# Performance work log

Hardware: AMD Instinct MI355X
Metric: run time of the kernel (lower is better)

The kernel has to match this reference:

```python
import jax, jax.numpy as jnp
import numpy as np

H, W = 512, 512
N = H * W
NCLS = 4
D_BI, D_SP = 5, 2
THETA_ALPHA, THETA_BETA, THETA_GAMMA = 80.0, 0.0625, 3.0
BI_COMPAT, SP_COMPAT, COMPATIBILITY = 10.0, 3.0, -1.0
NUM_ITER = 10


def _build_lattice(feats):
    """Permutohedral lattice precompute (numpy, integer index construction).
    feats: [N, d]. Returns os [N,d+1] int32 (1-based), ws [N,d+1] float32,
    bn [d+1, M, 2] int32 (0 = missing neighbor), M."""
    feats = np.asarray(feats, np.float64)
    n, d = feats.shape
    inv_std = np.sqrt(2.0 / 3.0) * (d + 1)
    scale = inv_std / np.sqrt((np.arange(d) + 1.0) * (np.arange(d) + 2.0))
    cf = feats * scale
    # embedding matrix E: elevated = cf @ E.T lies on the hyperplane sum=0
    E = np.zeros((d + 1, d))
    E[0, :] = 1.0
    for j in range(1, d + 1):
        E[j, j:] = 1.0
        E[j, j - 1] = -j
    elevated = cf @ E.T  # [n, d+1]
    greedy = (np.rint(elevated / (d + 1)) * (d + 1)).astype(np.int64)
    diff = elevated - greedy
    idx = np.arange(d + 1)
    upper = idx[None, :] > idx[:, None]
    lower = idx[None, :] < idx[:, None]
    di = diff[:, :, None]
    dj = diff[:, None, :]
    rank = (((dj > di) & upper) | ((dj >= di) & lower)).sum(-1)
    rank = rank + greedy.sum(1, keepdims=True) // (d + 1)
    low = rank < 0
    rank = rank + np.where(low, d + 1, 0)
    greedy = greedy + np.where(low, d + 1, 0)
    high = rank > d
    rank = rank - np.where(high, d + 1, 0)
    greedy = greedy - np.where(high, d + 1, 0)
    # barycentric weights
    bary = np.zeros((n, d + 2))
    v = (elevated - greedy) / (d + 1)
    rows = np.repeat(np.arange(n), d + 1)
    np.add.at(bary, (rows, (d - rank).ravel()), v.ravel())
    np.add.at(bary, (rows, (d + 1 - rank).ravel()), -v.ravel())
    bary[:, 0] += 1.0 + bary[:, d + 1]
    ws = bary[:, : d + 1].astype(np.float32)
    # simplex vertex keys (first d coords; last is implied by zero-sum)
    keys = np.empty((n, d + 1, d), np.int64)
    for r in range(d + 1):
        keys[:, r, :] = (greedy + r - (d + 1) * (rank > d - r))[:, :d]
    flat = keys.reshape(-1, d)
    lo = flat.min(0) - (d + 1)
    hi = flat.max(0) + (d + 1)
    strides = np.cumprod(np.concatenate([[1], (hi - lo + 1)[:-1]]))
    coords = (flat - lo) @ strides
    uniq, first, inv = np.unique(coords, return_index=True, return_inverse=True)
    M = int(len(uniq))
    os_ = (inv.reshape(n, d + 1) + 1).astype(np.int32)
    ukeys = flat[first]
    bn = np.zeros((d + 1, M, 2), np.int32)
    for j in range(d + 1):
        n1 = ukeys - 1
        n2 = ukeys + 1
        if j < d:
            n1[:, j] = ukeys[:, j] + d
            n2[:, j] = ukeys[:, j] - d
        for t, nk in enumerate((n1, n2)):
            c = (nk - lo) @ strides
            pos = np.clip(np.searchsorted(uniq, c), 0, M - 1)
            bn[j, :, t] = np.where(uniq[pos] == c, pos + 1, 0)
    return os_, ws, bn, M


def setup_inputs() -> dict:
    key = jax.random.key(0)
    k1, k2 = jax.random.split(key)
    image = jax.random.uniform(k1, (H, W, 7), dtype=jnp.float32)
    unary = jax.random.normal(k2, (H, W, NCLS), dtype=jnp.float32)
    img = np.asarray(image)
    yy, xx = np.mgrid[0:H, 0:W].astype(np.float64)
    bifeat = np.concatenate(
        [(xx / THETA_ALPHA)[..., None], (yy / THETA_ALPHA)[..., None],
         img[..., :3] / THETA_BETA], axis=-1).reshape(N, D_BI)
    spfeat = np.stack([xx / THETA_GAMMA, yy / THETA_GAMMA], -1).reshape(N, D_SP)
    os_b, ws_b, bn_b, M_b = _build_lattice(bifeat)
    os_s, ws_s, bn_s, M_s = _build_lattice(spfeat)
    return {
        "unary": unary,
        "ws_bilateral": jnp.asarray(ws_b), "os_bilateral": jnp.asarray(os_b),
        "blur_neighbors_bilateral": jnp.asarray(bn_b), "M_bilateral": M_b,
        "ws_spatial": jnp.asarray(ws_s), "os_spatial": jnp.asarray(os_s),
        "blur_neighbors_spatial": jnp.asarray(bn_s), "M_spatial": M_s,
    }


def _perm_filter(values, os_, ws, bn, M, alpha):
    # values: [N, C]; splat -> blur -> slice
    d1 = os_.shape[1]
    C = values.shape[1]
    table = jnp.zeros((M + 1, C), values.dtype)  # row 0 = dummy (missing)
    table = table.at[os_.reshape(-1)].add(
        (values[:, None, :] * ws[:, :, None]).reshape(-1, C))
    for j in range(d1):  # [0.5, 1, 0.5] blur along each lattice axis
        table = table.at[1:].add(0.5 * (table[bn[j, :, 0]] + table[bn[j, :, 1]]))
    return alpha * jnp.einsum("nrc,nr->nc", table[os_], ws)


def _mean_field(unary, ws_b, os_b, bn_b, M_b, ws_s, os_s, bn_s, M_s):
    C = unary.shape[-1]
    u = unary.reshape(N, C)
    alpha_b = 1.0 / (1.0 + 2.0 ** (-D_BI))
    alpha_s = 1.0 / (1.0 + 2.0 ** (-D_SP))
    ones = jnp.ones((N, 1), u.dtype)
    inv_nb = 1.0 / (_perm_filter(ones, os_b, ws_b, bn_b, M_b, alpha_b) + 1e-20)
    inv_ns = 1.0 / (_perm_filter(ones, os_s, ws_s, bn_s, M_s, alpha_s) + 1e-20)
    Q = jax.nn.softmax(-u, axis=-1)
    for _ in range(NUM_ITER):
        msg = (BI_COMPAT * _perm_filter(Q, os_b, ws_b, bn_b, M_b, alpha_b) * inv_nb
               + SP_COMPAT * _perm_filter(Q, os_s, ws_s, bn_s, M_s, alpha_s) * inv_ns)
        Q = jax.nn.softmax(-u - COMPATIBILITY * msg, axis=-1)
    return Q.reshape(H, W, C)


def reference(unary, ws_bilateral, os_bilateral, blur_neighbors_bilateral, M_bilateral,
              ws_spatial, os_spatial, blur_neighbors_spatial, M_spatial):
    # Returns the refined marginals Q [H, W, NCLS]; the module's MAP output is
    # jnp.argmax(Q, -1) (kept soft here so fwd/bwd share one output).
    return _mean_field(unary, ws_bilateral, os_bilateral, blur_neighbors_bilateral,
                       M_bilateral, ws_spatial, os_spatial, blur_neighbors_spatial,
                       M_spatial)
```

## Files before the change

### kernel.cpp

```cpp
#include <hip/hip_runtime.h>

#define NPIX (512 * 512)
#define BLK 256

#define SCAN_T 256
#define SCAN_E 8
#define SCAN_CHUNK (SCAN_T * SCAN_E)

typedef _Float16 h4 __attribute__((ext_vector_type(4)));

constexpr float ALPHA_B = 32.0f / 33.0f;
constexpr float ALPHA_S = 0.8f;
constexpr float BI_COMPAT = 10.0f;
constexpr float SP_COMPAT = 3.0f;

__device__ __forceinline__ unsigned pack_ent(int n, float w) {
    float wc = fminf(fmaxf(w, 0.f), 1.f);
    unsigned iw = (unsigned)(wc * 16383.f + 0.5f);
    return (iw << 18) | (unsigned)n;
}
__device__ __forceinline__ int ent_pix(unsigned e) { return (int)(e & 0x3FFFFu); }
__device__ __forceinline__ float ent_w(unsigned e) {
    return (float)(e >> 18) * (1.0f / 16383.0f);
}

__device__ __forceinline__ float4 f4zero() { return make_float4(0.f, 0.f, 0.f, 0.f); }
__device__ __forceinline__ h4 h4zero() {
    h4 z; z.x = (_Float16)0.f; z.y = (_Float16)0.f; z.z = (_Float16)0.f; z.w = (_Float16)0.f;
    return z;
}

__global__ void k_softmax_init(const float4* __restrict__ u, float4* __restrict__ Q) {
    int n = blockIdx.x * BLK + threadIdx.x;
    if (n >= NPIX) return;
    float4 uu = u[n];
    float l0 = -uu.x, l1 = -uu.y, l2 = -uu.z, l3 = -uu.w;
    float m = fmaxf(fmaxf(l0, l1), fmaxf(l2, l3));
    float e0 = expf(l0 - m), e1 = expf(l1 - m), e2 = expf(l2 - m), e3 = expf(l3 - m);
    float inv = 1.0f / (e0 + e1 + e2 + e3);
    Q[n] = make_float4(e0 * inv, e1 * inv, e2 * inv, e3 * inv);
}

__global__ void k_count_softmax(const int* __restrict__ osb, const int* __restrict__ oss,
                                int* __restrict__ cntB, int* __restrict__ cntS,
                                const float4* __restrict__ u, float4* __restrict__ Q) {
    int n = blockIdx.x * BLK + threadIdx.x;
    if (n >= NPIX) return;
    float4 uu = u[n];
    float l0 = -uu.x, l1 = -uu.y, l2 = -uu.z, l3 = -uu.w;
    float m = fmaxf(fmaxf(l0, l1), fmaxf(l2, l3));
    float e0 = expf(l0 - m), e1 = expf(l1 - m), e2 = expf(l2 - m), e3 = expf(l3 - m);
    float inv = 1.0f / (e0 + e1 + e2 + e3);
    Q[n] = make_float4(e0 * inv, e1 * inv, e2 * inv, e3 * inv);
#pragma unroll
    for (int r = 0; r < 6; r++) atomicAdd(&cntB[osb[n * 6 + r]], 1);
#pragma unroll
    for (int r = 0; r < 3; r++) atomicAdd(&cntS[oss[n * 3 + r]], 1);
}

__global__ void k_chunk_sum(const int* __restrict__ counts, int V, int* __restrict__ csum) {
    __shared__ int lds[SCAN_T];
    int base = blockIdx.x * SCAN_CHUNK;
    int s = 0;
#pragma unroll
    for (int j = 0; j < SCAN_E; j++) {
        int idx = base + threadIdx.x * SCAN_E + j;
        if (idx < V) s += counts[idx];
    }
    lds[threadIdx.x] = s;
    __syncthreads();
    for (int off = SCAN_T / 2; off > 0; off >>= 1) {
        if ((int)threadIdx.x < off) lds[threadIdx.x] += lds[threadIdx.x + off];
        __syncthreads();
    }
    if (threadIdx.x == 0) csum[blockIdx.x] = lds[0];
}

__global__ void k_scan_csum(int* __restrict__ csum, int nchunks) {
    __shared__ int lds[SCAN_T];
    int carry = 0;
    for (int base = 0; base < nchunks; base += SCAN_T) {
        int idx = base + threadIdx.x;
        int v = (idx < nchunks) ? csum[idx] : 0;
        lds[threadIdx.x] = v;
        __syncthreads();
        for (int off = 1; off < SCAN_T; off <<= 1) {
            int t = ((int)threadIdx.x >= off) ? lds[threadIdx.x - off] : 0;
            __syncthreads();
            lds[threadIdx.x] += t;
            __syncthreads();
        }
        int incl = lds[threadIdx.x];
        int tile_total = lds[SCAN_T - 1];
        if (idx < nchunks) csum[idx] = incl - v + carry;
        carry += tile_total;
        __syncthreads();
    }
}

__global__ void k_chunk_scan(const int* __restrict__ counts, int V,
                             const int* __restrict__ csum, int* __restrict__ start,
                             int* __restrict__ cursor) {
    __shared__ int lds[SCAN_T];
    int base = blockIdx.x * SCAN_CHUNK;
    int local[SCAN_E];
    int s = 0;
#pragma unroll
    for (int j = 0; j < SCAN_E; j++) {
        int idx = base + threadIdx.x * SCAN_E + j;
        int c = (idx < V) ? counts[idx] : 0;
        local[j] = c;
        s += c;
    }
    lds[threadIdx.x] = s;
    __syncthreads();
    for (int off = 1; off < SCAN_T; off <<= 1) {
        int t = ((int)threadIdx.x >= off) ? lds[threadIdx.x - off] : 0;
        __syncthreads();
        lds[threadIdx.x] += t;
        __syncthreads();
    }
    int excl = lds[threadIdx.x] - s + csum[blockIdx.x];
#pragma unroll
    for (int j = 0; j < SCAN_E; j++) {
        int idx = base + threadIdx.x * SCAN_E + j;
        if (idx < V) { start[idx] = excl; cursor[idx] = excl; }
        excl += local[j];
    }
}

__global__ void k_fill_both(const int* __restrict__ osb, const float* __restrict__ wsb,
                            int* __restrict__ curB, unsigned* __restrict__ entB,
                            const int* __restrict__ oss, const float* __restrict__ wss,
                            int* __restrict__ curS, unsigned* __restrict__ entS) {
    int n = blockIdx.x * BLK + threadIdx.x;
    if (n >= NPIX) return;
#pragma unroll
    for (int r = 0; r < 6; r++) {
        int o = osb[n * 6 + r];
        int pos = atomicAdd(&curB[o], 1);
        entB[pos] = pack_ent(n, wsb[n * 6 + r]);
    }
#pragma unroll
    for (int r = 0; r < 3; r++) {
        int o = oss[n * 3 + r];
        int pos = atomicAdd(&curS[o], 1);
        entS[pos] = pack_ent(n, wss[n * 3 + r]);
    }
}

__global__ void k_gather1_both(const unsigned* __restrict__ entB, const int* __restrict__ startB,
                               int totB, int Vb, float* __restrict__ nB,
                               const unsigned* __restrict__ entS, const int* __restrict__ startS,
                               int totS, int Vs, float* __restrict__ nS) {
    int i = blockIdx.x * BLK + threadIdx.x;
    const unsigned* ent; const int* st; int tot, V, idx; float* out;
    if (i < Vb) { ent = entB; st = startB; tot = totB; V = Vb; out = nB; idx = i; }
    else {
        idx = i - Vb;
        if (idx >= Vs) return;
        ent = entS; st = startS; tot = totS; V = Vs; out = nS;
    }
    int s = st[idx];
    int e = (idx + 1 < V) ? st[idx + 1] : tot;
    float acc = 0.f;
    for (int k = s; k < e; k++) acc += ent_w(ent[k]);
    out[idx] = acc;
}

__global__ void k_gather4h_both(const unsigned* __restrict__ entB, const int* __restrict__ startB,
                                int totB, int Vb, h4* __restrict__ tB,
                                const unsigned* __restrict__ entS, const int* __restrict__ startS,
                                int totS, int Vs, h4* __restrict__ tS,
                                const float4* __restrict__ Q) {
    int i = blockIdx.x * BLK + threadIdx.x;
    const unsigned* ent; const int* st; int tot, V, idx; h4* out;
    if (i < Vb) { ent = entB; st = startB; tot = totB; V = Vb; out = tB; idx = i; }
    else {
        idx = i - Vb;
        if (idx >= Vs) return;
        ent = entS; st = startS; tot = totS; V = Vs; out = tS;
    }
    int s = st[idx];
    int e = (idx + 1 < V) ? st[idx + 1] : tot;
    float ax = 0.f, ay = 0.f, az = 0.f, aw = 0.f;
    for (int k = s; k < e; k++) {
        unsigned en = ent[k];
        float w = ent_w(en);
        float4 q = Q[ent_pix(en)];
        ax += w * q.x; ay += w * q.y; az += w * q.z; aw += w * q.w;
    }
    h4 h;
    h.x = (_Float16)ax; h.y = (_Float16)ay; h.z = (_Float16)az; h.w = (_Float16)aw;
    out[idx] = h;
}

__global__ void k_blur1(const float* __restrict__ in, float* __restrict__ out,
                        const int* __restrict__ bn, int M) {
    int i = blockIdx.x * BLK + threadIdx.x;
    if (i > M) return;
    if (i == 0) { out[0] = 0.f; return; }
    int n1 = bn[(size_t)(i - 1) * 2 + 0];
    int n2 = bn[(size_t)(i - 1) * 2 + 1];
    out[i] = in[i] + 0.5f * (in[n1] + in[n2]);
}

__global__ void k_blur1_both(const float* __restrict__ inB, float* __restrict__ outB,
                             const int* __restrict__ bnB, int Mb,
                             const float* __restrict__ inS, float* __restrict__ outS,
                             const int* __restrict__ bnS, int Ms) {
    int i = blockIdx.x * BLK + threadIdx.x;
    const float* in; float* out; const int* bn; int M, idx;
    if (i <= Mb) { in = inB; out = outB; bn = bnB; M = Mb; idx = i; }
    else {
        idx = i - (Mb + 1);
        if (idx > Ms) return;
        in = inS; out = outS; bn = bnS; M = Ms;
    }
    if (idx == 0) { out[0] = 0.f; return; }
    int n1 = bn[(size_t)(idx - 1) * 2 + 0];
    int n2 = bn[(size_t)(idx - 1) * 2 + 1];
    out[idx] = in[idx] + 0.5f * (in[n1] + in[n2]);
}

__global__ void k_blur4h(const h4* __restrict__ in, h4* __restrict__ out,
                         const int* __restrict__ bn, int M) {
    int i = blockIdx.x * BLK + threadIdx.x;
    if (i > M) return;
    if (i == 0) { out[0] = h4zero(); return; }
    int n1 = bn[(size_t)(i - 1) * 2 + 0];
    int n2 = bn[(size_t)(i - 1) * 2 + 1];
    h4 a = in[i], b = in[n1], c = in[n2];
    h4 o;
    o.x = (_Float16)((float)a.x + 0.5f * ((float)b.x + (float)c.x));
    o.y = (_Float16)((float)a.y + 0.5f * ((float)b.y + (float)c.y));
    o.z = (_Float16)((float)a.z + 0.5f * ((float)b.z + (float)c.z));
    o.w = (_Float16)((float)a.w + 0.5f * ((float)b.w + (float)c.w));
    out[i] = o;
}

__global__ void k_blur4h_both(const h4* __restrict__ inB, h4* __restrict__ outB,
                              const int* __restrict__ bnB, int Mb,
                              const h4* __restrict__ inS, h4* __restrict__ outS,
                              const int* __restrict__ bnS, int Ms) {
    int i = blockIdx.x * BLK + threadIdx.x;
    const h4* in; h4* out; const int* bn; int M, idx;
    if (i <= Mb) { in = inB; out = outB; bn = bnB; M = Mb; idx = i; }
    else {
        idx = i - (Mb + 1);
        if (idx > Ms) return;
        in = inS; out = outS; bn = bnS; M = Ms;
    }
    if (idx == 0) { out[0] = h4zero(); return; }
    int n1 = bn[(size_t)(idx - 1) * 2 + 0];
    int n2 = bn[(size_t)(idx - 1) * 2 + 1];
    h4 a = in[idx], b = in[n1], c = in[n2];
    h4 o;
    o.x = (_Float16)((float)a.x + 0.5f * ((float)b.x + (float)c.x));
    o.y = (_Float16)((float)a.y + 0.5f * ((float)b.y + (float)c.y));
    o.z = (_Float16)((float)a.z + 0.5f * ((float)b.z + (float)c.z));
    o.w = (_Float16)((float)a.w + 0.5f * ((float)b.w + (float)c.w));
    out[idx] = o;
}

__global__ void k_norm_prescale(const float* __restrict__ nTb, const float* __restrict__ wsb,
                                const int* __restrict__ osb,
                                const float* __restrict__ nTs, const float* __restrict__ wss,
                                const int* __restrict__ oss,
                                float* __restrict__ wsbp, float* __restrict__ wssp) {
    int n = blockIdx.x * BLK + threadIdx.x;
    if (n >= NPIX) return;
    float sb = 0.f;
#pragma unroll
    for (int r = 0; r < 6; r++) sb += wsb[n * 6 + r] * nTb[osb[n * 6 + r]];
    float cb = BI_COMPAT * ALPHA_B / (ALPHA_B * sb + 1e-20f);
#pragma unroll
    for (int r = 0; r < 6; r++) wsbp[n * 6 + r] = wsb[n * 6 + r] * cb;
    float ss = 0.f;
#pragma unroll
    for (int r = 0; r < 3; r++) ss += wss[n * 3 + r] * nTs[oss[n * 3 + r]];
    float cs = SP_COMPAT * ALPHA_S / (ALPHA_S * ss + 1e-20f);
#pragma unroll
    for (int r = 0; r < 3; r++) wssp[n * 3 + r] = wss[n * 3 + r] * cs;
}

__global__ void k_slice_combine_h(const float4* __restrict__ u,
                                  const h4* __restrict__ tb, const float* __restrict__ wsbp,
                                  const int* __restrict__ osb,
                                  const h4* __restrict__ ts, const float* __restrict__ wssp,
                                  const int* __restrict__ oss,
                                  float4* __restrict__ Qout) {
    int n = blockIdx.x * BLK + threadIdx.x;
    if (n >= NPIX) return;
    float4 uu = u[n];
    float l0 = -uu.x, l1 = -uu.y, l2 = -uu.z, l3 = -uu.w;
#pragma unroll
    for (int r = 0; r < 6; r++) {
        float w = wsbp[n * 6 + r];
        h4 t = tb[osb[n * 6 + r]];
        l0 += w * (float)t.x; l1 += w * (float)t.y; l2 += w * (float)t.z; l3 += w * (float)t.w;
    }
#pragma unroll
    for (int r = 0; r < 3; r++) {
        float w = wssp[n * 3 + r];
        h4 t = ts[oss[n * 3 + r]];
        l0 += w * (float)t.x; l1 += w * (float)t.y; l2 += w * (float)t.z; l3 += w * (float)t.w;
    }
    float m = fmaxf(fmaxf(l0, l1), fmaxf(l2, l3));
    float e0 = expf(l0 - m), e1 = expf(l1 - m), e2 = expf(l2 - m), e3 = expf(l3 - m);
    float inv = 1.0f / (e0 + e1 + e2 + e3);
    Qout[n] = make_float4(e0 * inv, e1 * inv, e2 * inv, e3 * inv);
}

template <int D1>
__global__ void k_splat1(const float* __restrict__ ws, const int* __restrict__ os,
                         float* __restrict__ table) {
    int n = blockIdx.x * BLK + threadIdx.x;
    if (n >= NPIX) return;
#pragma unroll
    for (int r = 0; r < D1; r++) atomicAdd(&table[os[n * D1 + r]], ws[n * D1 + r]);
}

template <int D1>
__global__ void k_splat4(const float4* __restrict__ Q, const float* __restrict__ ws,
                         const int* __restrict__ os, float* __restrict__ table) {
    int n = blockIdx.x * BLK + threadIdx.x;
    if (n >= NPIX) return;
    float4 q = Q[n];
#pragma unroll
    for (int r = 0; r < D1; r++) {
        float w = ws[n * D1 + r];
        int o = os[n * D1 + r];
        float* t = table + 4 * (size_t)o;
        atomicAdd(t + 0, q.x * w);
        atomicAdd(t + 1, q.y * w);
        atomicAdd(t + 2, q.z * w);
        atomicAdd(t + 3, q.w * w);
    }
}

__global__ void k_blur4(const float4* __restrict__ in, float4* __restrict__ out,
                        const int* __restrict__ bn, int M) {
    int i = blockIdx.x * BLK + threadIdx.x;
    if (i > M) return;
    if (i == 0) { out[0] = f4zero(); return; }
    int n1 = bn[(size_t)(i - 1) * 2 + 0];
    int n2 = bn[(size_t)(i - 1) * 2 + 1];
    float4 a = in[i], b = in[n1], c = in[n2];
    out[i] = make_float4(a.x + 0.5f * (b.x + c.x), a.y + 0.5f * (b.y + c.y),
                         a.z + 0.5f * (b.z + c.z), a.w + 0.5f * (b.w + c.w));
}

template <int D1>
__global__ void k_norm_slice(const float* __restrict__ table, const float* __restrict__ ws,
                             const int* __restrict__ os, float alpha,
                             float* __restrict__ inv_out) {
    int n = blockIdx.x * BLK + threadIdx.x;
    if (n >= NPIX) return;
    float s = 0.f;
#pragma unroll
    for (int r = 0; r < D1; r++) s += ws[n * D1 + r] * table[os[n * D1 + r]];
    inv_out[n] = 1.0f / (alpha * s + 1e-20f);
}

__global__ void k_slice_combine(const float4* __restrict__ u,
                                const float4* __restrict__ tb, const float* __restrict__ wsb,
                                const int* __restrict__ osb,
                                const float4* __restrict__ ts, const float* __restrict__ wss,
                                const int* __restrict__ oss,
                                const float* __restrict__ inv_nb,
                                const float* __restrict__ inv_ns,
                                float4* __restrict__ Qout) {
    int n = blockIdx.x * BLK + threadIdx.x;
    if (n >= NPIX) return;
    float4 ab = f4zero();
#pragma unroll
    for (int r = 0; r < 6; r++) {
        float w = wsb[n * 6 + r];
        float4 t = tb[osb[n * 6 + r]];
        ab.x += w * t.x; ab.y += w * t.y; ab.z += w * t.z; ab.w += w * t.w;
    }
    float4 as = f4zero();
#pragma unroll
    for (int r = 0; r < 3; r++) {
        float w = wss[n * 3 + r];
        float4 t = ts[oss[n * 3 + r]];
        as.x += w * t.x; as.y += w * t.y; as.z += w * t.z; as.w += w * t.w;
    }
    float cb = BI_COMPAT * ALPHA_B * inv_nb[n];
    float cs = SP_COMPAT * ALPHA_S * inv_ns[n];
    float4 uu = u[n];
    float l0 = -uu.x + cb * ab.x + cs * as.x;
    float l1 = -uu.y + cb * ab.y + cs * as.y;
    float l2 = -uu.z + cb * ab.z + cs * as.z;
    float l3 = -uu.w + cb * ab.w + cs * as.w;
    float m = fmaxf(fmaxf(l0, l1), fmaxf(l2, l3));
    float e0 = expf(l0 - m), e1 = expf(l1 - m), e2 = expf(l2 - m), e3 = expf(l3 - m);
    float inv = 1.0f / (e0 + e1 + e2 + e3);
    Qout[n] = make_float4(e0 * inv, e1 * inv, e2 * inv, e3 * inv);
}

extern "C" void kernel_launch(void* const* d_in, const int* in_sizes, int n_in,
                              void* d_out, int out_size, void* d_ws, size_t ws_size,
                              hipStream_t stream) {
    const float* unary = (const float*)d_in[0];
    const float* wsb   = (const float*)d_in[1];
    const int*   osb   = (const int*)d_in[2];
    const int*   bnb   = (const int*)d_in[3];
    const float* wss   = (const float*)d_in[5];
    const int*   oss   = (const int*)d_in[6];
    const int*   bns   = (const int*)d_in[7];
    const int Mb = in_sizes[3] / 12;
    const int Ms = in_sizes[7] / 6;
    const int Vb = Mb + 1, Vs = Ms + 1;
    const int totB = NPIX * 6, totS = NPIX * 3;

    float* Q = (float*)d_out;

    char* p = (char*)d_ws;
    auto alloc = [&](size_t nbytes) -> void* {
        void* r = (void*)p;
        p += (nbytes + 15) & ~(size_t)15;
        return r;
    };
    h4*   tAb  = (h4*)alloc((size_t)Vb * 8);
    h4*   tBb  = (h4*)alloc((size_t)Vb * 8);
    h4*   tAs  = (h4*)alloc((size_t)Vs * 8);
    h4*   tBs  = (h4*)alloc((size_t)Vs * 8);
    float* nAb = (float*)alloc((size_t)Vb * 4);
    float* nBb = (float*)alloc((size_t)Vb * 4);
    float* nAs = (float*)alloc((size_t)Vs * 4);
    float* nBs = (float*)alloc((size_t)Vs * 4);
    float* wsbp = (float*)alloc((size_t)NPIX * 6 * 4);
    float* wssp = (float*)alloc((size_t)NPIX * 3 * 4);
    int*  startB  = (int*)alloc((size_t)Vb * 4);
    int*  cursorB = (int*)alloc((size_t)Vb * 4);
    unsigned* entB = (unsigned*)alloc((size_t)totB * 4);
    int*  startS  = (int*)alloc((size_t)Vs * 4);
    int*  cursorS = (int*)alloc((size_t)Vs * 4);
    unsigned* entS = (unsigned*)alloc((size_t)totS * 4);
    int*  csum    = (int*)alloc(8192 * 4);
    size_t need = (size_t)(p - (char*)d_ws);
    bool use_gather = need <= ws_size;

    dim3 blk(BLK);
    dim3 gN((NPIX + BLK - 1) / BLK);
    dim3 gVb((Vb + BLK - 1) / BLK);
    dim3 gVBS((Vb + Vs + BLK - 1) / BLK);

    if (use_gather) {
        int nchB = (Vb + SCAN_CHUNK - 1) / SCAN_CHUNK;
        int nchS = (Vs + SCAN_CHUNK - 1) / SCAN_CHUNK;
        hipMemsetAsync(cursorB, 0, (size_t)Vb * 4, stream);
        hipMemsetAsync(cursorS, 0, (size_t)Vs * 4, stream);
        k_count_softmax<<<gN, blk, 0, stream>>>(osb, oss, cursorB, cursorS,
                                                (const float4*)unary, (float4*)Q);
        k_chunk_sum<<<dim3(nchB), dim3(SCAN_T), 0, stream>>>(cursorB, Vb, csum);
        k_scan_csum<<<dim3(1), dim3(SCAN_T), 0, stream>>>(csum, nchB);
        k_chunk_scan<<<dim3(nchB), dim3(SCAN_T), 0, stream>>>(cursorB, Vb, csum, startB, cursorB);
        k_chunk_sum<<<dim3(nchS), dim3(SCAN_T), 0, stream>>>(cursorS, Vs, csum);
        k_scan_csum<<<dim3(1), dim3(SCAN_T), 0, stream>>>(csum, nchS);
        k_chunk_scan<<<dim3(nchS), dim3(SCAN_T), 0, stream>>>(cursorS, Vs, csum, startS, cursorS);
        k_fill_both<<<gN, blk, 0, stream>>>(osb, wsb, cursorB, entB, oss, wss, cursorS, entS);

        k_gather1_both<<<gVBS, blk, 0, stream>>>(entB, startB, totB, Vb, nAb,
                                                 entS, startS, totS, Vs, nAs);
        {
            float* a = nAb; float* b = nBb;
            float* as_ = nAs; float* bs_ = nBs;
            for (int j = 0; j < 3; j++) {
                k_blur1_both<<<gVBS, blk, 0, stream>>>(a, b, bnb + (size_t)j * Mb * 2, Mb,
                                                       as_, bs_, bns + (size_t)j * Ms * 2, Ms);
                float* t = a; a = b; b = t;
                t = as_; as_ = bs_; bs_ = t;
            }
            for (int j = 3; j < 6; j++) {
                k_blur1<<<gVb, blk, 0, stream>>>(a, b, bnb + (size_t)j * Mb * 2, Mb);
                float* t = a; a = b; b = t;
            }
            k_norm_prescale<<<gN, blk, 0, stream>>>(a, wsb, osb, as_, wss, oss, wsbp, wssp);
        }

        for (int it = 0; it < 10; it++) {
            k_gather4h_both<<<gVBS, blk, 0, stream>>>(entB, startB, totB, Vb, tAb,
                                                      entS, startS, totS, Vs, tAs,
                                                      (const float4*)Q);
            h4* a = tAb; h4* b = tBb;
            h4* as_ = tAs; h4* bs_ = tBs;
            for (int j = 0; j < 3; j++) {
                k_blur4h_both<<<gVBS, blk, 0, stream>>>(a, b, bnb + (size_t)j * Mb * 2, Mb,
                                                        as_, bs_, bns + (size_t)j * Ms * 2, Ms);
                h4* t = a; a = b; b = t;
                t = as_; as_ = bs_; bs_ = t;
            }
            for (int j = 3; j < 6; j++) {
                k_blur4h<<<gVb, blk, 0, stream>>>(a, b, bnb + (size_t)j * Mb * 2, Mb);
                h4* t = a; a = b; b = t;
            }
            k_slice_combine_h<<<gN, blk, 0, stream>>>((const float4*)unary,
                                                      a, wsbp, osb, as_, wssp, oss,
                                                      (float4*)Q);
        }
    } else {
        char* q = (char*)d_ws;
        auto alloc2 = [&](size_t nbytes) -> void* {
            void* r = (void*)q;
            q += (nbytes + 15) & ~(size_t)15;
            return r;
        };
        float* fAb = (float*)alloc2((size_t)Vb * 4 * sizeof(float));
        float* fBb = (float*)alloc2((size_t)Vb * 4 * sizeof(float));
        float* fAs = (float*)alloc2((size_t)Vs * 4 * sizeof(float));
        float* fBs = (float*)alloc2((size_t)Vs * 4 * sizeof(float));
        float* inv_nb = (float*)alloc2(NPIX * sizeof(float));
        float* inv_ns = (float*)alloc2(NPIX * sizeof(float));
        dim3 gMb((Mb + 1 + BLK - 1) / BLK);
        dim3 gMs((Ms + 1 + BLK - 1) / BLK);

        hipMemsetAsync(fAb, 0, (size_t)Vb * sizeof(float), stream);
        k_splat1<6><<<gN, blk, 0, stream>>>(wsb, osb, fAb);
        {
            float* a = fAb; float* b = fBb;
            for (int j = 0; j < 6; j++) {
                k_blur1<<<gMb, blk, 0, stream>>>(a, b, bnb + (size_t)j * Mb * 2, Mb);
                float* t = a; a = b; b = t;
            }
            k_norm_slice<6><<<gN, blk, 0, stream>>>(a, wsb, osb, ALPHA_B, inv_nb);
        }
        hipMemsetAsync(fAs, 0, (size_t)Vs * sizeof(float), stream);
        k_splat1<3><<<gN, blk, 0, stream>>>(wss, oss, fAs);
        {
            float* a = fAs; float* b = fBs;
            for (int j = 0; j < 3; j++) {
                k_blur1<<<gMs, blk, 0, stream>>>(a, b, bns + (size_t)j * Ms * 2, Ms);
                float* t = a; a = b; b = t;
            }
            k_norm_slice<3><<<gN, blk, 0, stream>>>(a, wss, oss, ALPHA_S, inv_ns);
        }
        k_softmax_init<<<gN, blk, 0, stream>>>((const float4*)unary, (float4*)Q);
        for (int it = 0; it < 10; it++) {
            hipMemsetAsync(fAb, 0, (size_t)Vb * 4 * sizeof(float), stream);
            k_splat4<6><<<gN, blk, 0, stream>>>((const float4*)Q, wsb, osb, fAb);
            float* a = fAb; float* b = fBb;
            for (int j = 0; j < 6; j++) {
                k_blur4<<<gMb, blk, 0, stream>>>((const float4*)a, (float4*)b,
                                                 bnb + (size_t)j * Mb * 2, Mb);
                float* t = a; a = b; b = t;
            }
            float* finb = a;
            hipMemsetAsync(fAs, 0, (size_t)Vs * 4 * sizeof(float), stream);
            k_splat4<3><<<gN, blk, 0, stream>>>((const float4*)Q, wss, oss, fAs);
            float* as_ = fAs; float* bs_ = fBs;
            for (int j = 0; j < 3; j++) {
                k_blur4<<<gMs, blk, 0, stream>>>((const float4*)as_, (float4*)bs_,
                                                 bns + (size_t)j * Ms * 2, Ms);
                float* t = as_; as_ = bs_; bs_ = t;
            }
            float* fins = as_;
            k_slice_combine<<<gN, blk, 0, stream>>>((const float4*)unary,
                                                    (const float4*)finb, wsb, osb,
                                                    (const float4*)fins, wss, oss,
                                                    inv_nb, inv_ns, (float4*)Q);
        }
    }
}
```

Before: 1.010 ms.

## Fuse pairs of lattice blur passes via recomputation and switch blur buffers to fp32

Each kernel now applies two consecutive per-axis blurs by recomputing the first blur at the neighbor vertices. The spatial lattice applies all three of its axes in a single kernel. This drops the blur launch count per iteration from six to three and removes the intermediate buffer round trips, at the cost of redundant gathers: three times the reads for a two-axis fuse and nine times for the spatial three-axis fuse. Lattice buffers also move from fp16 to fp32, which doubles their memory traffic but removes the conversion and rounding.

```diff
diff --git a/kernel.cpp b/kernel.cpp
--- a/kernel.cpp
+++ b/kernel.cpp
@@ -6,8 +6,6 @@
 #define SCAN_T 256
 #define SCAN_E 8
 #define SCAN_CHUNK (SCAN_T * SCAN_E)
-
-typedef _Float16 h4 __attribute__((ext_vector_type(4)));
 
 constexpr float ALPHA_B = 32.0f / 33.0f;
 constexpr float ALPHA_S = 0.8f;
@@ -25,9 +23,45 @@
 }
 
 __device__ __forceinline__ float4 f4zero() { return make_float4(0.f, 0.f, 0.f, 0.f); }
-__device__ __forceinline__ h4 h4zero() {
-    h4 z; z.x = (_Float16)0.f; z.y = (_Float16)0.f; z.z = (_Float16)0.f; z.w = (_Float16)0.f;
-    return z;
+
+__device__ __forceinline__ float4 f4_eval1(const float4* __restrict__ t,
+                                           const int* __restrict__ bn, int x) {
+    int b1 = bn[2 * (x - 1)], b2 = bn[2 * (x - 1) + 1];
+    float4 a = t[x], u = t[b1], v = t[b2];
+    return make_float4(a.x + 0.5f * (u.x + v.x),
+                       a.y + 0.5f * (u.y + v.y),
+                       a.z + 0.5f * (u.z + v.z),
+                       a.w + 0.5f * (u.w + v.w));
+}
+__device__ __forceinline__ float4 f4_eval2(const float4* __restrict__ t,
+                                           const int* __restrict__ bnA,
+                                           const int* __restrict__ bnB, int x) {
+    int a1 = bnB[2 * (x - 1)], a2 = bnB[2 * (x - 1) + 1];
+    float4 r = f4_eval1(t, bnA, x);
+    if (a1) {
+        float4 q = f4_eval1(t, bnA, a1);
+        r.x += 0.5f * q.x; r.y += 0.5f * q.y; r.z += 0.5f * q.z; r.w += 0.5f * q.w;
+    }
+    if (a2) {
+        float4 q = f4_eval1(t, bnA, a2);
+        r.x += 0.5f * q.x; r.y += 0.5f * q.y; r.z += 0.5f * q.z; r.w += 0.5f * q.w;
+    }
+    return r;
+}
+
+__device__ __forceinline__ float f_eval1(const float* __restrict__ t,
+                                         const int* __restrict__ bn, int x) {
+    int b1 = bn[2 * (x - 1)], b2 = bn[2 * (x - 1) + 1];
+    return t[x] + 0.5f * (t[b1] + t[b2]);
+}
+__device__ __forceinline__ float f_eval2(const float* __restrict__ t,
+                                         const int* __restrict__ bnA,
+                                         const int* __restrict__ bnB, int x) {
+    int a1 = bnB[2 * (x - 1)], a2 = bnB[2 * (x - 1) + 1];
+    float r = f_eval1(t, bnA, x);
+    if (a1) r += 0.5f * f_eval1(t, bnA, a1);
+    if (a2) r += 0.5f * f_eval1(t, bnA, a2);
+    return r;
 }
 
 __global__ void k_softmax_init(const float4* __restrict__ u, float4* __restrict__ Q) {
@@ -168,13 +202,13 @@
     out[idx] = acc;
 }
 
-__global__ void k_gather4h_both(const unsigned* __restrict__ entB, const int* __restrict__ startB,
-                                int totB, int Vb, h4* __restrict__ tB,
+__global__ void k_gather4f_both(const unsigned* __restrict__ entB, const int* __restrict__ startB,
+                                int totB, int Vb, float4* __restrict__ tB,
                                 const unsigned* __restrict__ entS, const int* __restrict__ startS,
-                                int totS, int Vs, h4* __restrict__ tS,
+                                int totS, int Vs, float4* __restrict__ tS,
                                 const float4* __restrict__ Q) {
     int i = blockIdx.x * BLK + threadIdx.x;
-    const unsigned* ent; const int* st; int tot, V, idx; h4* out;
+    const unsigned* ent; const int* st; int tot, V, idx; float4* out;
     if (i < Vb) { ent = entB; st = startB; tot = totB; V = Vb; out = tB; idx = i; }
     else {
         idx = i - Vb;
@@ -183,84 +217,82 @@
     }
     int s = st[idx];
     int e = (idx + 1 < V) ? st[idx + 1] : tot;
-    float ax = 0.f, ay = 0.f, az = 0.f, aw = 0.f;
+    float4 acc = f4zero();
     for (int k = s; k < e; k++) {
         unsigned en = ent[k];
         float w = ent_w(en);
         float4 q = Q[ent_pix(en)];
-        ax += w * q.x; ay += w * q.y; az += w * q.z; aw += w * q.w;
-    }
-    h4 h;
-    h.x = (_Float16)ax; h.y = (_Float16)ay; h.z = (_Float16)az; h.w = (_Float16)aw;
-    out[idx] = h;
-}
-
-__global__ void k_blur1(const float* __restrict__ in, float* __restrict__ out,
-                        const int* __restrict__ bn, int M) {
+        acc.x += w * q.x; acc.y += w * q.y; acc.z += w * q.z; acc.w += w * q.w;
+    }
+    out[idx] = acc;
+}
+
+__global__ void k_cblur4f_both(const float4* __restrict__ inB, float4* __restrict__ outB,
+                               const int* __restrict__ bnb, int Mb,
+                               const float4* __restrict__ inS, float4* __restrict__ outS,
+                               const int* __restrict__ bns, int Ms) {
+    int i = blockIdx.x * BLK + threadIdx.x;
+    if (i <= Mb) {
+        if (i == 0) { outB[0] = f4zero(); return; }
+        outB[i] = f4_eval2(inB, bnb, bnb + (size_t)Mb * 2, i);
+        return;
+    }
+    int idx = i - (Mb + 1);
+    if (idx > Ms) return;
+    if (idx == 0) { outS[0] = f4zero(); return; }
+    const int* sn0 = bns;
+    const int* sn1 = bns + (size_t)Ms * 2;
+    const int* sn2 = bns + (size_t)Ms * 4;
+    int c1 = sn2[2 * (idx - 1)], c2 = sn2[2 * (idx - 1) + 1];
+    float4 r = f4_eval2(inS, sn0, sn1, idx);
+    if (c1) {
+        float4 q = f4_eval2(inS, sn0, sn1, c1);
+        r.x += 0.5f * q.x; r.y += 0.5f * q.y; r.z += 0.5f * q.z; r.w += 0.5f * q.w;
+    }
+    if (c2) {
+        float4 q = f4_eval2(inS, sn0, sn1, c2);
+        r.x += 0.5f * q.x; r.y += 0.5f * q.y; r.z += 0.5f * q.z; r.w += 0.5f * q.w;
+    }
+    outS[idx] = r;
+}
+
+__global__ void k_cblur4f(const float4* __restrict__ in, float4* __restrict__ out,
+                          const int* __restrict__ bnA, const int* __restrict__ bnB_, int M) {
+    int i = blockIdx.x * BLK + threadIdx.x;
+    if (i > M) return;
+    if (i == 0) { out[0] = f4zero(); return; }
+    out[i] = f4_eval2(in, bnA, bnB_, i);
+}
+
+__global__ void k_cblur1_both(const float* __restrict__ inB, float* __restrict__ outB,
+                              const int* __restrict__ bnb, int Mb,
+                              const float* __restrict__ inS, float* __restrict__ outS,
+                              const int* __restrict__ bns, int Ms) {
+    int i = blockIdx.x * BLK + threadIdx.x;
+    if (i <= Mb) {
+        if (i == 0) { outB[0] = 0.f; return; }
+        outB[i] = f_eval2(inB, bnb, bnb + (size_t)Mb * 2, i);
+        return;
+    }
+    int idx = i - (Mb + 1);
+    if (idx > Ms) return;
+    if (idx == 0) { outS[0] = 0.f; return; }
+    const int* sn0 = bns;
+    const int* sn1 = bns + (size_t)Ms * 2;
+    const int* sn2 = bns + (size_t)Ms * 4;
+    int c1 = sn2[2 * (idx - 1)], c2 = sn2[2 * (idx - 1) + 1];
+    float r = f_eval2(inS, sn0, sn1, idx);
+    if (c1) r += 0.5f * f_eval2(inS, sn0, sn1, c1);
+    if (c2) r += 0.5f * f_eval2(inS, sn0, sn1, c2);
+    outS[idx] = r;
+}
+
+__global__ void k_cblur1(const float* __restrict__ in, float* __restrict__ out,
+                         const int* __restrict__ bnA, const int* __restrict__ bnB_, int M) {
     int i = blockIdx.x * BLK + threadIdx.x;
     if (i > M) return;
     if (i == 0) { out[0] = 0.f; return; }
-    int n1 = bn[(size_t)(i - 1) * 2 + 0];
-    int n2 = bn[(size_t)(i - 1) * 2 + 1];
-    out[i] = in[i] + 0.5f * (in[n1] + in[n2]);
-}
-
-__global__ void k_blur1_both(const float* __restrict__ inB, float* __restrict__ outB,
-                             const int* __restrict__ bnB, int Mb,
-                             const float* __restrict__ inS, float* __restrict__ outS,
-                             const int* __restrict__ bnS, int Ms) {
-    int i = blockIdx.x * BLK + threadIdx.x;
-    const float* in; float* out; const int* bn; int M, idx;
-    if (i <= Mb) { in = inB; out = outB; bn = bnB; M = Mb; idx = i; }
-    else {
-        idx = i - (Mb + 1);
-        if (idx > Ms) return;
-        in = inS; out = outS; bn = bnS; M = Ms;
-    }
-    if (idx == 0) { out[0] = 0.f; return; }
-    int n1 = bn[(size_t)(idx - 1) * 2 + 0];
-    int n2 = bn[(size_t)(idx - 1) * 2 + 1];
-    out[idx] = in[idx] + 0.5f * (in[n1] + in[n2]);
-}
-
-__global__ void k_blur4h(const h4* __restrict__ in, h4* __restrict__ out,
-                         const int* __restrict__ bn, int M) {
-    int i = blockIdx.x * BLK + threadIdx.x;
-    if (i > M) return;
-    if (i == 0) { out[0] = h4zero(); return; }
-    int n1 = bn[(size_t)(i - 1) * 2 + 0];
-    int n2 = bn[(size_t)(i - 1) * 2 + 1];
-    h4 a = in[i], b = in[n1], c = in[n2];
-    h4 o;
-    o.x = (_Float16)((float)a.x + 0.5f * ((float)b.x + (float)c.x));
-    o.y = (_Float16)((float)a.y + 0.5f * ((float)b.y + (float)c.y));
-    o.z = (_Float16)((float)a.z + 0.5f * ((float)b.z + (float)c.z));
-    o.w = (_Float16)((float)a.w + 0.5f * ((float)b.w + (float)c.w));
-    out[i] = o;
-}
-
-__global__ void k_blur4h_both(const h4* __restrict__ inB, h4* __restrict__ outB,
-                              const int* __restrict__ bnB, int Mb,
-                              const h4* __restrict__ inS, h4* __restrict__ outS,
-                              const int* __restrict__ bnS, int Ms) {
-    int i = blockIdx.x * BLK + threadIdx.x;
-    const h4* in; h4* out; const int* bn; int M, idx;
-    if (i <= Mb) { in = inB; out = outB; bn = bnB; M = Mb; idx = i; }
-    else {
-        idx = i - (Mb + 1);
-        if (idx > Ms) return;
-        in = inS; out = outS; bn = bnS; M = Ms;
-    }
-    if (idx == 0) { out[0] = h4zero(); return; }
-    int n1 = bn[(size_t)(idx - 1) * 2 + 0];
-    int n2 = bn[(size_t)(idx - 1) * 2 + 1];
-    h4 a = in[idx], b = in[n1], c = in[n2];
-    h4 o;
-    o.x = (_Float16)((float)a.x + 0.5f * ((float)b.x + (float)c.x));
-    o.y = (_Float16)((float)a.y + 0.5f * ((float)b.y + (float)c.y));
-    o.z = (_Float16)((float)a.z + 0.5f * ((float)b.z + (float)c.z));
-    o.w = (_Float16)((float)a.w + 0.5f * ((float)b.w + (float)c.w));
-    out[idx] = o;
+    out[i] = f_eval2(in, bnA, bnB_, i);
 }
 
 __global__ void k_norm_prescale(const float* __restrict__ nTb, const float* __restrict__ wsb,
@@ -284,10 +316,10 @@
     for (int r = 0; r < 3; r++) wssp[n * 3 + r] = wss[n * 3 + r] * cs;
 }
 
-__global__ void k_slice_combine_h(const float4* __restrict__ u,
-                                  const h4* __restrict__ tb, const float* __restrict__ wsbp,
+__global__ void k_slice_combine_f(const float4* __restrict__ u,
+                                  const float4* __restrict__ tb, const float* __restrict__ wsbp,
                                   const int* __restrict__ osb,
-                                  const h4* __restrict__ ts, const float* __restrict__ wssp,
+                                  const float4* __restrict__ ts, const float* __restrict__ wssp,
                                   const int* __restrict__ oss,
                                   float4* __restrict__ Qout) {
     int n = blockIdx.x * BLK + threadIdx.x;
@@ -297,14 +329,14 @@
 #pragma unroll
     for (int r = 0; r < 6; r++) {
         float w = wsbp[n * 6 + r];
-        h4 t = tb[osb[n * 6 + r]];
-        l0 += w * (float)t.x; l1 += w * (float)t.y; l2 += w * (float)t.z; l3 += w * (float)t.w;
+        float4 t = tb[osb[n * 6 + r]];
+        l0 += w * t.x; l1 += w * t.y; l2 += w * t.z; l3 += w * t.w;
     }
 #pragma unroll
     for (int r = 0; r < 3; r++) {
         float w = wssp[n * 3 + r];
-        h4 t = ts[oss[n * 3 + r]];
-        l0 += w * (float)t.x; l1 += w * (float)t.y; l2 += w * (float)t.z; l3 += w * (float)t.w;
+        float4 t = ts[oss[n * 3 + r]];
+        l0 += w * t.x; l1 += w * t.y; l2 += w * t.z; l3 += w * t.w;
     }
     float m = fmaxf(fmaxf(l0, l1), fmaxf(l2, l3));
     float e0 = expf(l0 - m), e1 = expf(l1 - m), e2 = expf(l2 - m), e3 = expf(l3 - m);
@@ -337,6 +369,16 @@
         atomicAdd(t + 2, q.z * w);
         atomicAdd(t + 3, q.w * w);
     }
+}
+
+__global__ void k_blur1(const float* __restrict__ in, float* __restrict__ out,
+                        const int* __restrict__ bn, int M) {
+    int i = blockIdx.x * BLK + threadIdx.x;
+    if (i > M) return;
+    if (i == 0) { out[0] = 0.f; return; }
+    int n1 = bn[(size_t)(i - 1) * 2 + 0];
+    int n2 = bn[(size_t)(i - 1) * 2 + 1];
+    out[i] = in[i] + 0.5f * (in[n1] + in[n2]);
 }
 
 __global__ void k_blur4(const float4* __restrict__ in, float4* __restrict__ out,
@@ -423,10 +465,10 @@
         p += (nbytes + 15) & ~(size_t)15;
         return r;
     };
-    h4*   tAb  = (h4*)alloc((size_t)Vb * 8);
-    h4*   tBb  = (h4*)alloc((size_t)Vb * 8);
-    h4*   tAs  = (h4*)alloc((size_t)Vs * 8);
-    h4*   tBs  = (h4*)alloc((size_t)Vs * 8);
+    float4* tAb = (float4*)alloc((size_t)Vb * 16);
+    float4* tBb = (float4*)alloc((size_t)Vb * 16);
+    float4* tAs = (float4*)alloc((size_t)Vs * 16);
+    float4* tBs = (float4*)alloc((size_t)Vs * 16);
     float* nAb = (float*)alloc((size_t)Vb * 4);
     float* nBb = (float*)alloc((size_t)Vb * 4);
     float* nAs = (float*)alloc((size_t)Vs * 4);
@@ -448,6 +490,11 @@
     dim3 gVb((Vb + BLK - 1) / BLK);
     dim3 gVBS((Vb + Vs + BLK - 1) / BLK);
 
+    const int* bnb2 = bnb + (size_t)2 * Mb * 2;
+    const int* bnb3 = bnb + (size_t)3 * Mb * 2;
+    const int* bnb4 = bnb + (size_t)4 * Mb * 2;
+    const int* bnb5 = bnb + (size_t)5 * Mb * 2;
+
     if (use_gather) {
         int nchB = (Vb + SCAN_CHUNK - 1) / SCAN_CHUNK;
         int nchS = (Vs + SCAN_CHUNK - 1) / SCAN_CHUNK;
@@ -465,40 +512,20 @@
 
         k_gather1_both<<<gVBS, blk, 0, stream>>>(entB, startB, totB, Vb, nAb,
                                                  entS, startS, totS, Vs, nAs);
-        {
-            float* a = nAb; float* b = nBb;
-            float* as_ = nAs; float* bs_ = nBs;
-            for (int j = 0; j < 3; j++) {
-                k_blur1_both<<<gVBS, blk, 0, stream>>>(a, b, bnb + (size_t)j * Mb * 2, Mb,
-                                                       as_, bs_, bns + (size_t)j * Ms * 2, Ms);
-                float* t = a; a = b; b = t;
-                t = as_; as_ = bs_; bs_ = t;
-            }
-            for (int j = 3; j < 6; j++) {
-                k_blur1<<<gVb, blk, 0, stream>>>(a, b, bnb + (size_t)j * Mb * 2, Mb);
-                float* t = a; a = b; b = t;
-            }
-            k_norm_prescale<<<gN, blk, 0, stream>>>(a, wsb, osb, as_, wss, oss, wsbp, wssp);
-        }
+        k_cblur1_both<<<gVBS, blk, 0, stream>>>(nAb, nBb, bnb, Mb, nAs, nBs, bns, Ms);
+        k_cblur1<<<gVb, blk, 0, stream>>>(nBb, nAb, bnb2, bnb3, Mb);
+        k_cblur1<<<gVb, blk, 0, stream>>>(nAb, nBb, bnb4, bnb5, Mb);
+        k_norm_prescale<<<gN, blk, 0, stream>>>(nBb, wsb, osb, nBs, wss, oss, wsbp, wssp);
 
         for (int it = 0; it < 10; it++) {
-            k_gather4h_both<<<gVBS, blk, 0, stream>>>(entB, startB, totB, Vb, tAb,
+            k_gather4f_both<<<gVBS, blk, 0, stream>>>(entB, startB, totB, Vb, tAb,
                                                       entS, startS, totS, Vs, tAs,
                                                       (const float4*)Q);
-            h4* a = tAb; h4* b = tBb;
-            h4* as_ = tAs; h4* bs_ = tBs;
-            for (int j = 0; j < 3; j++) {
-                k_blur4h_both<<<gVBS, blk, 0, stream>>>(a, b, bnb + (size_t)j * Mb * 2, Mb,
-                                                        as_, bs_, bns + (size_t)j * Ms * 2, Ms);
-                h4* t = a; a = b; b = t;
-                t = as_; as_ = bs_; bs_ = t;
-            }
-            for (int j = 3; j < 6; j++) {
-                k_blur4h<<<gVb, blk, 0, stream>>>(a, b, bnb + (size_t)j * Mb * 2, Mb);
-                h4* t = a; a = b; b = t;
-            }
-            k_slice_combine_h<<<gN, blk, 0, stream>>>((const float4*)unary,
-                                                      a, wsbp, osb, as_, wssp, oss,
+            k_cblur4f_both<<<gVBS, blk, 0, stream>>>(tAb, tBb, bnb, Mb, tAs, tBs, bns, Ms);
+            k_cblur4f<<<gVb, blk, 0, stream>>>(tBb, tAb, bnb2, bnb3, Mb);
+            k_cblur4f<<<gVb, blk, 0, stream>>>(tAb, tBb, bnb4, bnb5, Mb);
+            k_slice_combine_f<<<gN, blk, 0, stream>>>((const float4*)unary,
+                                                      tBb, wsbp, osb, tBs, wssp, oss,
                                                       (float4*)Q);
         }
     } else {
```

Measured after the change: 1.019 ms. About the same (+0.8%).
